# Kernel optimization log

Hardware: AMD Instinct MI355X
Metric: run time of the kernel (lower is better)

The kernel has to match this reference:

```python
import jax, jax.numpy as jnp
import numpy as np

B, N, NODE_DIM = 256, 200, 2
H, D, L, FF = 8, 128, 3, 512
KD = D // H  # key/val dim per head = 16
EPS = 1e-5


def _uniform(key, shape, fan):
    s = 1.0 / np.sqrt(fan)
    return jax.random.uniform(key, shape, jnp.float32, -s, s)


def setup_inputs() -> dict:
    key = jax.random.key(0)
    ks = jax.random.split(key, 16)
    return {
        "x": jax.random.normal(ks[0], (B, N, NODE_DIM), jnp.float32),
        "Wemb": _uniform(ks[1], (NODE_DIM, D), NODE_DIM),
        "bemb": _uniform(ks[2], (D,), NODE_DIM),
        "Wq": _uniform(ks[3], (L, H, D, KD), KD),
        "Wk": _uniform(ks[4], (L, H, D, KD), KD),
        "Wv": _uniform(ks[5], (L, H, D, KD), KD),
        "Wo": _uniform(ks[6], (L, H, KD, D), D),
        "bn1_g": jnp.ones((L, D), jnp.float32),
        "bn1_b": jnp.zeros((L, D), jnp.float32),
        "W1": _uniform(ks[7], (L, D, FF), D),
        "b1": _uniform(ks[8], (L, FF), D),
        "W2": _uniform(ks[9], (L, FF, D), FF),
        "b2": _uniform(ks[10], (L, D), FF),
        "bn2_g": jnp.ones((L, D), jnp.float32),
        "bn2_b": jnp.zeros((L, D), jnp.float32),
    }


def _batch_norm(h, g, b):
    # BatchNorm1d in training mode: stats over all (batch*graph) positions per channel
    hf = h.reshape(-1, h.shape[-1])
    m = hf.mean(axis=0)
    v = hf.var(axis=0)  # biased variance, as torch uses for normalization
    return (h - m) * jax.lax.rsqrt(v + EPS) * g + b


def _mha(h, Wq, Wk, Wv, Wo):
    # h: [B,N,D]; Wq/Wk/Wv: [H,D,KD]; Wo: [H,KD,D]
    Q = jnp.einsum('bnd,hdk->hbnk', h, Wq)
    K = jnp.einsum('bnd,hdk->hbnk', h, Wk)
    V = jnp.einsum('bnd,hdk->hbnk', h, Wv)
    scores = jnp.einsum('hbqk,hbnk->hbqn', Q, K) * (1.0 / np.sqrt(KD))
    attn = jax.nn.softmax(scores, axis=-1)
    heads = jnp.einsum('hbqn,hbnk->hbqk', attn, V)
    return jnp.einsum('hbqk,hkd->bqd', heads, Wo)


def reference(x, Wemb, bemb, Wq, Wk, Wv, Wo, bn1_g, bn1_b, W1, b1, W2, b2, bn2_g, bn2_b):
    h = x @ Wemb + bemb  # init_embed: [B,N,D]
    for l in range(L):
        h = h + _mha(h, Wq[l], Wk[l], Wv[l], Wo[l])
        h = _batch_norm(h, bn1_g[l], bn1_b[l])
        ff = jax.nn.relu(h @ W1[l] + b1[l]) @ W2[l] + b2[l]
        h = _batch_norm(h + ff, bn2_g[l], bn2_b[l])
    return (h, h.mean(axis=1))
```

## Files before the change

### kernel.cpp

```cpp
#include <hip/hip_runtime.h>
#include <math.h>

#define B_ 256
#define N_ 200
#define D_ 128
#define H_ 8
#define KD_ 16
#define L_ 3
#define FF_ 512
#define ROWS (B_*N_)
#define BND (ROWS*D_)

typedef float f32x4 __attribute__((ext_vector_type(4)));
typedef _Float16 f16x4 __attribute__((ext_vector_type(4)));
typedef _Float16 f16x8 __attribute__((ext_vector_type(8)));

__device__ __forceinline__ ushort f2h_bits(float f) {
  _Float16 h = (_Float16)f;
  union { _Float16 h; ushort u; } v; v.h = h; return v.u;
}
__device__ __forceinline__ float h2f(ushort u) {
  union { ushort u; _Float16 h; } v; v.u = u; return (float)v.h;
}
__device__ __forceinline__ void bn_reduce(const float* psum, const float* psq,
    const float* gamma, const float* beta, int c, float& sc, float& sh) {
  if (gamma == nullptr) { sc = 1.f; sh = 0.f; return; }
  float s = psum[c], q = psq[c];
  const float invM = 1.f / 51200.f;
  float m = s * invM;
  float v = fmaf(q, invM, -m * m);
  float rr = rsqrtf(v + 1e-5f);
  sc = rr * gamma[c];
  sh = fmaf(-m, sc, beta[c]);
}

__global__ __launch_bounds__(256) void init_kernel(const float* __restrict__ x,
    const float* __restrict__ Wemb, const float* __restrict__ bemb,
    const float* __restrict__ Wo, const float* __restrict__ W2,
    ushort* __restrict__ h, ushort* __restrict__ woT, ushort* __restrict__ w2T,
    float* __restrict__ pa_s, float* __restrict__ pa_q,
    float* __restrict__ pb_s, float* __restrict__ pb_q)
{
  int blk = blockIdx.x, t = threadIdx.x;
  if (blk < 6400) {
    int i4 = blk * 256 + t;
    int r  = i4 >> 5, c4 = i4 & 31;
    float x0 = x[2*r], x1 = x[2*r + 1];
    const float4 w0 = ((const float4*)Wemb)[c4];
    const float4 w1 = ((const float4*)Wemb)[32 + c4];
    const float4 bb = ((const float4*)bemb)[c4];
    ushort o16[4];
    o16[0] = f2h_bits(fmaf(x0, w0.x, fmaf(x1, w1.x, bb.x)));
    o16[1] = f2h_bits(fmaf(x0, w0.y, fmaf(x1, w1.y, bb.y)));
    o16[2] = f2h_bits(fmaf(x0, w0.z, fmaf(x1, w1.z, bb.z)));
    o16[3] = f2h_bits(fmaf(x0, w0.w, fmaf(x1, w1.w, bb.w)));
    uint2 p;
    p.x = (uint)o16[0] | ((uint)o16[1] << 16);
    p.y = (uint)o16[2] | ((uint)o16[3] << 16);
    ((uint2*)h)[i4] = p;
  } else if (blk < 7360) {
    int i = (blk - 6400) * 256 + t;
    if (i < 49152) {
      int l = i / 16384, r = i % 16384;
      int n = r >> 7, k = r & 127;
      int hh = k >> 4, kd = k & 15;
      woT[i] = f2h_bits(Wo[l*16384 + hh*2048 + kd*128 + n]);
    } else {
      int j = i - 49152;
      int l = j / 65536, r = j % 65536;
      int d = r >> 9, f = r & 511;
      w2T[j] = f2h_bits(W2[l*65536 + f*128 + d]);
    }
  } else {
    if (t < 128) { pa_s[t] = 0.f; pa_q[t] = 0.f; pb_s[t] = 0.f; pb_q[t] = 0.f; }
  }
}

__global__ __launch_bounds__(128) void fold_qkv(const float* __restrict__ Wq,
    const float* __restrict__ Wk, const float* __restrict__ Wv,
    const float* __restrict__ pb_s, const float* __restrict__ pb_q,
    const float* __restrict__ gamma, const float* __restrict__ beta,
    ushort* __restrict__ wh, float* __restrict__ bout,
    float* __restrict__ scout, float* __restrict__ shout,
    float* __restrict__ pa_s, float* __restrict__ pa_q)
{
  __shared__ float wsum[2];
  int n = blockIdx.x;
  int k = threadIdx.x;
  float sc, sh;
  bn_reduce(pb_s, pb_q, gamma, beta, k, sc, sh);
  if (n == 0) { scout[k] = sc; shout[k] = sh; }
  if (n == 1) { pa_s[k] = 0.f; pa_q[k] = 0.f; }
  int which = n >> 7, hh = (n >> 4) & 7, kd = n & 15;
  const float* src = (which == 0) ? Wq : (which == 1) ? Wk : Wv;
  float w = src[hh*2048 + k*16 + kd];
  if (which == 0) w *= 0.25f * 1.44269504088896340736f;
  wh[n*128 + k] = f2h_bits(w * sc);
  float p = sh * w;
#pragma unroll
  for (int d = 1; d < 64; d <<= 1) p += __shfl_xor(p, d);
  if ((k & 63) == 0) wsum[k >> 6] = p;
  __syncthreads();
  if (k == 0) bout[n] = wsum[0] + wsum[1];
}

__global__ __launch_bounds__(128) void fold_w1(const float* __restrict__ W1,
    const float* __restrict__ b1,
    const float* __restrict__ pa_s, const float* __restrict__ pa_q,
    const float* __restrict__ gamma, const float* __restrict__ beta,
    ushort* __restrict__ wh, float* __restrict__ bout,
    float* __restrict__ scout, float* __restrict__ shout)
{
  __shared__ float wsum[2];
  int f = blockIdx.x;
  int k = threadIdx.x;
  float sc, sh;
  bn_reduce(pa_s, pa_q, gamma, beta, k, sc, sh);
  if (f == 0) { scout[k] = sc; shout[k] = sh; }
  float w = W1[k*512 + f];
  wh[f*128 + k] = f2h_bits(w * sc);
  float p = sh * w;
#pragma unroll
  for (int d = 1; d < 64; d <<= 1) p += __shfl_xor(p, d);
  if ((k & 63) == 0) wsum[k >> 6] = p;
  __syncthreads();
  if (k == 0) bout[f] = b1[f] + wsum[0] + wsum[1];
}

template<int K, bool BIAS, bool RELU, bool RESIDBN,
         bool OUTQKV, bool OUT16, bool STATS>
__global__ __launch_bounds__(256, 2) void gemm_mfma(
    const ushort* __restrict__ Ah,
    const ushort* __restrict__ Wh,
    const float* __restrict__ bias,
    const ushort* rh,
    const float* __restrict__ rsc, const float* __restrict__ rsh,
    ushort* o0, ushort* o1, ushort* o2,
    float* __restrict__ psum, float* __restrict__ psq, int Ntot)
{
  __shared__ ushort AhS[128*64];
  __shared__ ushort BhS[128*64];
  const int t    = threadIdx.x;
  const int nx   = gridDim.x;
  const int nwg  = nx * gridDim.y;
  const int lin  = blockIdx.y * nx + blockIdx.x;
  const int q8   = nwg >> 3, r8 = nwg & 7;
  const int xcd  = lin & 7, i8 = lin >> 3;
  const int wg   = (xcd < r8 ? xcd*(q8+1) : r8*(q8+1) + (xcd-r8)*q8) + i8;
  const int bm   = (wg / nx) * 128;
  const int bn   = (wg % nx) * 128;
  const int lane = t & 63;
  const int w    = t >> 6, wm = w >> 1, wn = w & 1;
  const int quad = lane >> 4, l15 = lane & 15;

  f32x4 acc[4][4];
#pragma unroll
  for (int i = 0; i < 4; i++)
#pragma unroll
    for (int j = 0; j < 4; j++) acc[i][j] = (f32x4){0.f, 0.f, 0.f, 0.f};

  const ushort* AhB = Ah + (size_t)bm * K;
  const ushort* BhB = Wh + (size_t)bn * K;

  for (int k0 = 0; k0 < K; k0 += 64) {
#pragma unroll
    for (int i = 0; i < 4; i++) {
      int idx = i * 256 + t;
      int row = idx >> 3, c = idx & 7;
      int k8  = c ^ (row & 7);
      size_t off = (size_t)row * K + k0 + k8 * 8;
      ((uint4*)AhS)[idx] = *(const uint4*)(AhB + off);
      ((uint4*)BhS)[idx] = *(const uint4*)(BhB + off);
    }
    __syncthreads();
#pragma unroll
    for (int ks = 0; ks < 2; ks++) {
      f16x8 ah[4], bh[4];
#pragma unroll
      for (int i = 0; i < 4; i++) {
        int row = wm * 64 + i * 16 + l15;
        int k8  = ks * 4 + quad;
        int ci  = k8 ^ (row & 7);
        ah[i] = ((const f16x8*)AhS)[row * 8 + ci];
        int nrow = wn * 64 + i * 16 + l15;
        int cj   = k8 ^ (nrow & 7);
        bh[i] = ((const f16x8*)BhS)[nrow * 8 + cj];
      }
#pragma unroll
      for (int i = 0; i < 4; i++)
#pragma unroll
        for (int j = 0; j < 4; j++)
          acc[i][j] = __builtin_amdgcn_mfma_f32_16x16x32_f16(ah[i], bh[j], acc[i][j], 0, 0, 0);
    }
    __syncthreads();
  }

  float bv[4], scv[4], shv[4];
#pragma unroll
  for (int j = 0; j < 4; j++) {
    int col = bn + wn*64 + j*16 + l15;
    if (BIAS)    bv[j]  = bias[col];
    if (RESIDBN) { scv[j] = rsc[col]; shv[j] = rsh[col]; }
  }
  float sj[4] = {0.f,0.f,0.f,0.f}, qj[4] = {0.f,0.f,0.f,0.f};
#pragma unroll
  for (int i = 0; i < 4; i++) {
#pragma unroll
    for (int r = 0; r < 4; r++) {
      int row = bm + wm*64 + i*16 + quad*4 + r;
#pragma unroll
      for (int j = 0; j < 4; j++) {
        int col = bn + wn*64 + j*16 + l15;
        float v = acc[i][j][r];
        if (BIAS)    v += bv[j];
        if (RELU)    v = fmaxf(v, 0.f);
        if (RESIDBN) {
          float rr = h2f(rh[(size_t)row * Ntot + col]);
          v += fmaf(rr, scv[j], shv[j]);
        }
        if (OUTQKV) {
          if (bn == 0) {
            o0[((size_t)(col >> 4) * ROWS + row) * 16 + (col & 15)] = f2h_bits(v);
          } else if (bn == 128) {
            int c = col - 128;
            o1[((size_t)(c >> 4) * ROWS + row) * 16 + (c & 15)] = f2h_bits(v);
          } else {
            int c = col - 256;
            o2[((size_t)(c >> 4) * ROWS + row) * 16 + (c & 15)] = f2h_bits(v);
          }
        }
        if (OUT16) o0[(size_t)row * Ntot + col] = f2h_bits(v);
        if (STATS) { sj[j] += v; qj[j] = fmaf(v, v, qj[j]); }
      }
    }
  }
  if (STATS) {
#pragma unroll
    for (int j = 0; j < 4; j++) {
      sj[j] += __shfl_xor(sj[j], 16); sj[j] += __shfl_xor(sj[j], 32);
      qj[j] += __shfl_xor(qj[j], 16); qj[j] += __shfl_xor(qj[j], 32);
    }
    float* ssum = (float*)AhS;
    float* ssq  = ssum + 128;
    if (t < 128) { ssum[t] = 0.f; ssq[t] = 0.f; }
    __syncthreads();
    if (quad == 0) {
#pragma unroll
      for (int j = 0; j < 4; j++) {
        int col = wn*64 + j*16 + l15;
        atomicAdd(&ssum[col], sj[j]);
        atomicAdd(&ssq[col],  qj[j]);
      }
    }
    __syncthreads();
    if (t < 128) {
      atomicAdd(&psum[t], ssum[t]);
      atomicAdd(&psq[t],  ssq[t]);
    }
  }
}

__global__ __launch_bounds__(256) void attn_kernel(const ushort* __restrict__ qs,
    const ushort* __restrict__ ks, const ushort* __restrict__ vh,
    ushort* __restrict__ hd, float* __restrict__ pb_s, float* __restrict__ pb_q)
{
  __shared__ __align__(16) _Float16 Ksh[208*24];
  __shared__ __align__(16) _Float16 VTh[16*216];
  const int b  = blockIdx.x >> 3;
  const int hh = blockIdx.x & 7;
  const int t  = threadIdx.x;
  if (blockIdx.x == 0 && t < 128) { pb_s[t] = 0.f; pb_q[t] = 0.f; }
  const size_t rb = (size_t)b * N_;
  const size_t hb = ((size_t)hh * ROWS + rb) * 16;

  for (int i = t; i < 208*2; i += 256) {
    int n = i >> 1, half = i & 1;
    uint4 kv = {0u, 0u, 0u, 0u};
    if (n < N_) kv = *(const uint4*)(ks + hb + n*16 + half*8);
    *(uint4*)&Ksh[n*24 + half*8] = kv;
  }
  for (int i = t; i < 208*2; i += 256) {
    int n = i >> 1, half = i & 1;
    uint4 v0 = {0u, 0u, 0u, 0u};
    if (n < N_) v0 = *(const uint4*)(vh + hb + n*16 + half*8);
    const ushort* e0 = (const ushort*)&v0;
#pragma unroll
    for (int q = 0; q < 8; q++)
      ((ushort*)VTh)[(half*8 + q)*216 + n] = e0[q];
  }
  __syncthreads();

  const int lane = t & 63;
  const int w    = t >> 6;
  const int l15  = lane & 15;
  const int g    = lane >> 4;

  for (int qt = w; qt < 13; qt += 4) {
    int qr  = qt*16 + l15;
    int qrc = qr < N_ ? qr : N_-1;
    f16x4 bq = *(const f16x4*)(qs + hb + (size_t)qrc*16 + g*4);

    f32x4 ct[13];
#pragma unroll
    for (int kt = 0; kt < 13; kt++) {
      f16x4 ak = *(const f16x4*)&Ksh[(kt*16 + l15)*24 + g*4];
      ct[kt] = __builtin_amdgcn_mfma_f32_16x16x16f16(ak, bq, (f32x4){0.f,0.f,0.f,0.f}, 0, 0, 0);
    }
#pragma unroll
    for (int r = 0; r < 4; r++)
      if (g*4 + r >= 8) ct[12][r] = -1e30f;

    float m0 = -1e30f, m1 = -1e30f;
#pragma unroll
    for (int kt = 0; kt < 13; kt++) {
      m0 = fmaxf(m0, fmaxf(ct[kt][0], ct[kt][1]));
      m1 = fmaxf(m1, fmaxf(ct[kt][2], ct[kt][3]));
    }
    float m = fmaxf(m0, m1);
    m = fmaxf(m, __shfl_xor(m, 16));
    m = fmaxf(m, __shfl_xor(m, 32));

    float la0 = 0.f, la1 = 0.f, la2 = 0.f, la3 = 0.f;
#pragma unroll
    for (int kt = 0; kt < 13; kt++) {
      float p0 = __builtin_amdgcn_exp2f(ct[kt][0] - m);
      float p1 = __builtin_amdgcn_exp2f(ct[kt][1] - m);
      float p2 = __builtin_amdgcn_exp2f(ct[kt][2] - m);
      float p3 = __builtin_amdgcn_exp2f(ct[kt][3] - m);
      la0 += p0; la1 += p1; la2 += p2; la3 += p3;
      ct[kt][0] = p0; ct[kt][1] = p1; ct[kt][2] = p2; ct[kt][3] = p3;
    }
    float l = (la0 + la1) + (la2 + la3);
    l += __shfl_xor(l, 16);
    l += __shfl_xor(l, 32);

    f32x4 och = {0.f,0.f,0.f,0.f};
#pragma unroll
    for (int kt = 0; kt < 13; kt++) {
      f16x4 pt = { (_Float16)ct[kt][0], (_Float16)ct[kt][1],
                   (_Float16)ct[kt][2], (_Float16)ct[kt][3] };
      f16x4 avh = *(const f16x4*)&VTh[l15*216 + kt*16 + g*4];
      och = __builtin_amdgcn_mfma_f32_16x16x16f16(avh, pt, och, 0, 0, 0);
    }

    if (qr < N_) {
      float inv = __builtin_amdgcn_rcpf(l);
      ushort o16[4];
#pragma unroll
      for (int r = 0; r < 4; r++) o16[r] = f2h_bits(och[r] * inv);
      uint2 p;
      p.x = (uint)o16[0] | ((uint)o16[1] << 16);
      p.y = (uint)o16[2] | ((uint)o16[3] << 16);
      *(uint2*)(hd + (rb + qr)*128 + hh*16 + g*4) = p;
    }
  }
}

__global__ __launch_bounds__(256) void bn_mean_final(const ushort* __restrict__ h,
    const float* __restrict__ pb_s, const float* __restrict__ pb_q,
    const float* __restrict__ gamma, const float* __restrict__ beta,
    float* __restrict__ outh, float* __restrict__ mout)
{
  __shared__ float part[2][128];
  int b = blockIdx.x;
  int t = threadIdx.x;
  int d = t & 127, half = t >> 7;
  float sc, sh;
  bn_reduce(pb_s, pb_q, gamma, beta, d, sc, sh);
  float s = 0.f;
  for (int n = half*100; n < half*100 + 100; n++) {
    size_t idx = ((size_t)b * N_ + n) * 128 + d;
    float v = fmaf(h2f(h[idx]), sc, sh);
    outh[idx] = v;
    s += v;
  }
  part[half][d] = s;
  __syncthreads();
  if (half == 0) mout[b * 128 + d] = (part[0][d] + part[1][d]) * (1.f / N_);
}

extern "C" void kernel_launch(void* const* d_in, const int* in_sizes, int n_in,
                              void* d_out, int out_size, void* d_ws, size_t ws_size,
                              hipStream_t stream)
{
  const float* x    = (const float*)d_in[0];
  const float* Wemb = (const float*)d_in[1];
  const float* bemb = (const float*)d_in[2];
  const float* Wq   = (const float*)d_in[3];
  const float* Wk   = (const float*)d_in[4];
  const float* Wv   = (const float*)d_in[5];
  const float* Wo   = (const float*)d_in[6];
  const float* bn1g = (const float*)d_in[7];
  const float* bn1b = (const float*)d_in[8];
  const float* W1   = (const float*)d_in[9];
  const float* b1   = (const float*)d_in[10];
  const float* W2   = (const float*)d_in[11];
  const float* b2   = (const float*)d_in[12];
  const float* bn2g = (const float*)d_in[13];
  const float* bn2b = (const float*)d_in[14];
  float* out = (float*)d_out;

  char* wsb = (char*)d_ws;
  ushort* h     = (ushort*)wsb;
  char*   phase = wsb + 13107200;
  ushort* qsb   = (ushort*)phase;
  ushort* ksb   = (ushort*)(phase + 13107200);
  ushort* vhh   = (ushort*)(phase + 26214400);
  ushort* hd    = (ushort*)(phase + 52428800);
  ushort* hid   = (ushort*)phase;
  char*   wp    = wsb + 78643200;
  ushort* woT   = (ushort*)wp;
  ushort* w2T   = (ushort*)(wp + 98304);
  ushort* fqkvw = (ushort*)(wp + 491520);
  ushort* fw1w  = (ushort*)(wp + 589824);
  float*  fqkv_b = (float*)(wp + 720896);
  float*  fw1_b  = (float*)(wp + 722432);
  float*  pa_s   = (float*)(wp + 724480);
  float*  pa_q   = (float*)(wp + 724992);
  float*  pb_s   = (float*)(wp + 725504);
  float*  pb_q   = (float*)(wp + 726016);
  float*  sc_a   = (float*)(wp + 726528);
  float*  sh_a   = (float*)(wp + 727040);
  float*  sc_b   = (float*)(wp + 727552);
  float*  sh_b   = (float*)(wp + 728064);

  init_kernel<<<7361, 256, 0, stream>>>(x, Wemb, bemb, Wo, W2, h, woT, w2T,
                                        pa_s, pa_q, pb_s, pb_q);

  for (int l = 0; l < L_; l++) {
    fold_qkv<<<384, 128, 0, stream>>>(Wq + l*16384, Wk + l*16384, Wv + l*16384,
                                      pb_s, pb_q,
                                      l == 0 ? nullptr : bn2g + (l-1)*128,
                                      l == 0 ? nullptr : bn2b + (l-1)*128,
                                      fqkvw, fqkv_b, sc_b, sh_b, pa_s, pa_q);
    gemm_mfma<128, true, false, false, true, false, false>
        <<<dim3(3, 400), 256, 0, stream>>>(
        h, fqkvw, fqkv_b, nullptr, nullptr, nullptr,
        qsb, ksb, vhh, nullptr, nullptr, 384);
    attn_kernel<<<B_ * H_, 256, 0, stream>>>(qsb, ksb, vhh, hd, pb_s, pb_q);
    gemm_mfma<128, false, false, true, false, true, true>
        <<<dim3(1, 400), 256, 0, stream>>>(
        hd, woT + l*16384, nullptr, h, sc_b, sh_b,
        h, nullptr, nullptr, pa_s, pa_q, 128);
    fold_w1<<<512, 128, 0, stream>>>(W1 + l*65536, b1 + l*512,
                                     pa_s, pa_q, bn1g + l*128, bn1b + l*128,
                                     fw1w, fw1_b, sc_a, sh_a);
    gemm_mfma<128, true, true, false, false, true, false>
        <<<dim3(4, 400), 256, 0, stream>>>(
        h, fw1w, fw1_b, nullptr, nullptr, nullptr,
        hid, nullptr, nullptr, nullptr, nullptr, 512);
    gemm_mfma<512, true, false, true, false, true, true>
        <<<dim3(1, 400), 256, 0, stream>>>(
        hid, w2T + l*65536, b2 + l*128, h, sc_a, sh_a,
        h, nullptr, nullptr, pb_s, pb_q, 128);
  }

  bn_mean_final<<<B_, 256, 0, stream>>>(h, pb_s, pb_q,
                                        bn2g + 2*128, bn2b + 2*128, out, out + BND);
}
```

Before: 527.7 us.

## Fuse FFN up- and down-projection GEMMs into one kernel keeping hidden tile in LDS

Replaces the two FFN GEMM launches (W1 with ReLU writing a 512-wide hidden activation to global memory, then W2 reading it back) with a single kernel. Each 128-row block loops over four 128-wide hidden chunks, computes relu(h·W1+b1) into shared memory and immediately accumulates it into the W2 output. The same kernel also applies the residual with BN scale/shift and accumulates BN statistics. This removes the global round trip of the hidden tensor and one launch, but there are only 400 blocks at one block per CU with about 96KB of LDS each, so per-CU occupancy is low and weight loads are not double-buffered.

After: 552.1 us. 4.6% more time.

```diff
diff --git a/kernel.cpp b/kernel.cpp
--- a/kernel.cpp
+++ b/kernel.cpp
@@ -260,6 +260,187 @@
   }
 }
 
+__global__ __launch_bounds__(256, 1) void ffn_fused(
+    const ushort* __restrict__ h,
+    const ushort* __restrict__ w1,
+    const float* __restrict__ b1f,
+    const ushort* __restrict__ w2t,
+    const float* __restrict__ b2,
+    const float* __restrict__ rsc, const float* __restrict__ rsh,
+    ushort* hout,
+    float* __restrict__ psum, float* __restrict__ psq)
+{
+  __shared__ ushort Ash[2*128*64];
+  __shared__ ushort WB [2*128*64];
+  __shared__ ushort HB [2*128*72];
+  const int t    = threadIdx.x;
+  const int bm   = blockIdx.x * 128;
+  const int lane = t & 63;
+  const int w    = t >> 6, wm = w >> 1, wn = w & 1;
+  const int quad = lane >> 4, l15 = lane & 15;
+
+  {
+    const ushort* AB = h + (size_t)bm * 128;
+    for (int half = 0; half < 2; half++)
+#pragma unroll
+      for (int i = 0; i < 4; i++) {
+        int idx = i * 256 + t;
+        int row = idx >> 3, c = idx & 7;
+        int k8  = c ^ (row & 7);
+        ((uint4*)(Ash + half*8192))[idx] = *(const uint4*)(AB + (size_t)row*128 + half*64 + k8*8);
+      }
+  }
+
+  f32x4 aco[4][4];
+#pragma unroll
+  for (int i = 0; i < 4; i++)
+#pragma unroll
+    for (int j = 0; j < 4; j++) aco[i][j] = (f32x4){0.f, 0.f, 0.f, 0.f};
+
+  __syncthreads();
+
+  for (int ch = 0; ch < 4; ch++) {
+    {
+      const ushort* W1B = w1 + (size_t)ch * 128 * 128;
+      for (int half = 0; half < 2; half++)
+#pragma unroll
+        for (int i = 0; i < 4; i++) {
+          int idx = i * 256 + t;
+          int row = idx >> 3, c = idx & 7;
+          int k8  = c ^ (row & 7);
+          ((uint4*)(WB + half*8192))[idx] = *(const uint4*)(W1B + (size_t)row*128 + half*64 + k8*8);
+        }
+    }
+    __syncthreads();
+    f32x4 ach[4][4];
+#pragma unroll
+    for (int i = 0; i < 4; i++)
+#pragma unroll
+      for (int j = 0; j < 4; j++) ach[i][j] = (f32x4){0.f, 0.f, 0.f, 0.f};
+#pragma unroll
+    for (int ks = 0; ks < 4; ks++) {
+      int half = ks >> 1, k8 = (ks & 1)*4 + quad;
+      f16x8 ah[4], bh[4];
+#pragma unroll
+      for (int i = 0; i < 4; i++) {
+        int row = wm*64 + i*16 + l15;
+        int ci  = k8 ^ (row & 7);
+        ah[i] = ((const f16x8*)(Ash + half*8192))[row*8 + ci];
+        int fr = wn*64 + i*16 + l15;
+        int cj  = k8 ^ (fr & 7);
+        bh[i] = ((const f16x8*)(WB + half*8192))[fr*8 + cj];
+      }
+#pragma unroll
+      for (int i = 0; i < 4; i++)
+#pragma unroll
+        for (int j = 0; j < 4; j++)
+          ach[i][j] = __builtin_amdgcn_mfma_f32_16x16x32_f16(ah[i], bh[j], ach[i][j], 0, 0, 0);
+    }
+    __syncthreads();
+    {
+      float bv1[4];
+#pragma unroll
+      for (int j = 0; j < 4; j++) bv1[j] = b1f[ch*128 + wn*64 + j*16 + l15];
+#pragma unroll
+      for (int i = 0; i < 4; i++)
+#pragma unroll
+        for (int r = 0; r < 4; r++) {
+          int row = wm*64 + i*16 + quad*4 + r;
+#pragma unroll
+          for (int j = 0; j < 4; j++) {
+            float hv = fmaxf(ach[i][j][r] + bv1[j], 0.f);
+            int k6  = j*16 + l15;
+            int ci8 = (k6 >> 3) ^ (row & 7);
+            HB[(wn*128 + row)*72 + ci8*8 + (l15 & 7)] = f2h_bits(hv);
+          }
+        }
+    }
+    {
+      const ushort* W2B = w2t + ch * 128;
+      for (int half = 0; half < 2; half++)
+#pragma unroll
+        for (int i = 0; i < 4; i++) {
+          int idx = i * 256 + t;
+          int row = idx >> 3, c = idx & 7;
+          int k8  = c ^ (row & 7);
+          ((uint4*)(WB + half*8192))[idx] = *(const uint4*)(W2B + (size_t)row*512 + half*64 + k8*8);
+        }
+    }
+    __syncthreads();
+#pragma unroll
+    for (int ks = 0; ks < 4; ks++) {
+      int half = ks >> 1, k8 = (ks & 1)*4 + quad;
+      f16x8 ah[4], bh[4];
+#pragma unroll
+      for (int i = 0; i < 4; i++) {
+        int row = wm*64 + i*16 + l15;
+        int ci  = k8 ^ (row & 7);
+        ah[i] = *(const f16x8*)&HB[(half*128 + row)*72 + ci*8];
+        int dr = wn*64 + i*16 + l15;
+        int cj  = k8 ^ (dr & 7);
+        bh[i] = ((const f16x8*)(WB + half*8192))[dr*8 + cj];
+      }
+#pragma unroll
+      for (int i = 0; i < 4; i++)
+#pragma unroll
+        for (int j = 0; j < 4; j++)
+          aco[i][j] = __builtin_amdgcn_mfma_f32_16x16x32_f16(ah[i], bh[j], aco[i][j], 0, 0, 0);
+    }
+    __syncthreads();
+  }
+
+  float bv[4], scv[4], shv[4];
+#pragma unroll
+  for (int j = 0; j < 4; j++) {
+    int col = wn*64 + j*16 + l15;
+    bv[j]  = b2[col];
+    scv[j] = rsc[col]; shv[j] = rsh[col];
+  }
+  float sj[4] = {0.f,0.f,0.f,0.f}, qj[4] = {0.f,0.f,0.f,0.f};
+#pragma unroll
+  for (int i = 0; i < 4; i++) {
+#pragma unroll
+    for (int r = 0; r < 4; r++) {
+      int rloc = wm*64 + i*16 + quad*4 + r;
+      int row  = bm + rloc;
+#pragma unroll
+      for (int j = 0; j < 4; j++) {
+        int col = wn*64 + j*16 + l15;
+        float v = aco[i][j][r] + bv[j];
+        int k6 = col & 63, half = col >> 6;
+        int ci = (k6 >> 3) ^ (rloc & 7);
+        float rr = h2f(Ash[half*8192 + rloc*64 + ci*8 + (k6 & 7)]);
+        v += fmaf(rr, scv[j], shv[j]);
+        hout[(size_t)row * 128 + col] = f2h_bits(v);
+        sj[j] += v; qj[j] = fmaf(v, v, qj[j]);
+      }
+    }
+  }
+#pragma unroll
+  for (int j = 0; j < 4; j++) {
+    sj[j] += __shfl_xor(sj[j], 16); sj[j] += __shfl_xor(sj[j], 32);
+    qj[j] += __shfl_xor(qj[j], 16); qj[j] += __shfl_xor(qj[j], 32);
+  }
+  __syncthreads();
+  float* ssum = (float*)Ash;
+  float* ssq  = ssum + 128;
+  if (t < 128) { ssum[t] = 0.f; ssq[t] = 0.f; }
+  __syncthreads();
+  if (quad == 0) {
+#pragma unroll
+    for (int j = 0; j < 4; j++) {
+      int col = wn*64 + j*16 + l15;
+      atomicAdd(&ssum[col], sj[j]);
+      atomicAdd(&ssq[col],  qj[j]);
+    }
+  }
+  __syncthreads();
+  if (t < 128) {
+    atomicAdd(&psum[t], ssum[t]);
+    atomicAdd(&psq[t],  ssq[t]);
+  }
+}
+
 __global__ __launch_bounds__(256) void attn_kernel(const ushort* __restrict__ qs,
     const ushort* __restrict__ ks, const ushort* __restrict__ vh,
     ushort* __restrict__ hd, float* __restrict__ pb_s, float* __restrict__ pb_q)
@@ -406,9 +587,8 @@
   ushort* qsb   = (ushort*)phase;
   ushort* ksb   = (ushort*)(phase + 13107200);
   ushort* vhh   = (ushort*)(phase + 26214400);
-  ushort* hd    = (ushort*)(phase + 52428800);
-  ushort* hid   = (ushort*)phase;
-  char*   wp    = wsb + 78643200;
+  ushort* hd    = (ushort*)(phase + 39321600);
+  char*   wp    = wsb + 65536000;
   ushort* woT   = (ushort*)wp;
   ushort* w2T   = (ushort*)(wp + 98304);
   ushort* fqkvw = (ushort*)(wp + 491520);
@@ -445,14 +625,9 @@
     fold_w1<<<512, 128, 0, stream>>>(W1 + l*65536, b1 + l*512,
                                      pa_s, pa_q, bn1g + l*128, bn1b + l*128,
                                      fw1w, fw1_b, sc_a, sh_a);
-    gemm_mfma<128, true, true, false, false, true, false>
-        <<<dim3(4, 400), 256, 0, stream>>>(
-        h, fw1w, fw1_b, nullptr, nullptr, nullptr,
-        hid, nullptr, nullptr, nullptr, nullptr, 512);
-    gemm_mfma<512, true, false, true, false, true, true>
-        <<<dim3(1, 400), 256, 0, stream>>>(
-        hid, w2T + l*65536, b2 + l*128, h, sc_a, sh_a,
-        h, nullptr, nullptr, pb_s, pb_q, 128);
+    ffn_fused<<<400, 256, 0, stream>>>(
+        h, fw1w, fw1_b, w2T + l*65536, b2 + l*128, sc_a, sh_a,
+        h, pb_s, pb_q);
   }
 
   bn_mean_final<<<B_, 256, 0, stream>>>(h, pb_s, pb_q,
```

## Fuse FFN up- and down-projection GEMMs into one kernel keeping hidden in registers

Applied to the files above, without the earlier changes.

Replaces the two FFN GEMM launches (W1 with ReLU writing a 512-wide fp16 hidden buffer, then W2 with residual, BN-apply and stats) with a single kernel. Each block handles 64 rows, loops over four 128-wide hidden chunks, and stages swizzled W1 and W2 tiles in shared memory. The hidden activations stay in registers as fp16 MFMA operands and are never written to global memory. This saves the hidden tensor's write and read traffic and one launch, but weights are reloaded per 64-row block and reuse per block is lower, and the input h is read and written in place.

New measurement: 592.8 us. 1.12x slower.

```diff
diff --git a/kernel.cpp b/kernel.cpp
--- a/kernel.cpp
+++ b/kernel.cpp
@@ -260,6 +260,129 @@
   }
 }
 
+__global__ __launch_bounds__(256, 3) void ffn_fused(
+    const ushort* __restrict__ h,
+    const ushort* __restrict__ w1,
+    const float* __restrict__ b1f,
+    const ushort* __restrict__ w2t,
+    const float* __restrict__ b2,
+    const float* __restrict__ rsc, const float* __restrict__ rsh,
+    ushort* hout,
+    float* __restrict__ psum, float* __restrict__ psq)
+{
+  __shared__ ushort WB[128*128];
+  __shared__ float ssum[128], ssq[128];
+  const int t    = threadIdx.x;
+  const int bm   = blockIdx.x * 64;
+  const int lane = t & 63;
+  const int wv   = t >> 6;
+  const int quad = lane >> 4, l15 = lane & 15;
+  const int row  = bm + wv*16 + l15;
+
+  f16x4 bq[8];
+#pragma unroll
+  for (int ks = 0; ks < 8; ks++)
+    bq[ks] = *(const f16x4*)(h + (size_t)row*128 + ks*16 + quad*4);
+
+  if (t < 128) { ssum[t] = 0.f; ssq[t] = 0.f; }
+
+  f32x4 co[8];
+#pragma unroll
+  for (int dt = 0; dt < 8; dt++) co[dt] = (f32x4){0.f,0.f,0.f,0.f};
+
+  for (int ch = 0; ch < 4; ch++) {
+    __syncthreads();
+    {
+      const ushort* W1B = w1 + (size_t)ch*128*128;
+#pragma unroll
+      for (int i = 0; i < 8; i++) {
+        int idx = i*256 + t;
+        int r = idx >> 4, c = idx & 15;
+        int k8 = c ^ (r & 7);
+        ((uint4*)WB)[idx] = *(const uint4*)(W1B + (size_t)r*128 + k8*8);
+      }
+    }
+    __syncthreads();
+    f16x4 hb[8];
+#pragma unroll
+    for (int ft = 0; ft < 8; ft++) {
+      f32x4 hc = (f32x4){0.f,0.f,0.f,0.f};
+#pragma unroll
+      for (int ks = 0; ks < 8; ks++) {
+        int fr = ft*16 + l15;
+        int k  = ks*16 + quad*4;
+        int gi = (k >> 3) ^ (fr & 7);
+        f16x4 af = *(const f16x4*)&WB[fr*128 + gi*8 + (k & 7)];
+        hc = __builtin_amdgcn_mfma_f32_16x16x16f16(af, bq[ks], hc, 0, 0, 0);
+      }
+      float4 b1v = *(const float4*)(b1f + ch*128 + ft*16 + quad*4);
+      hb[ft] = (f16x4){
+        (_Float16)fmaxf(hc[0] + b1v.x, 0.f),
+        (_Float16)fmaxf(hc[1] + b1v.y, 0.f),
+        (_Float16)fmaxf(hc[2] + b1v.z, 0.f),
+        (_Float16)fmaxf(hc[3] + b1v.w, 0.f) };
+    }
+    __syncthreads();
+    {
+      const ushort* W2B = w2t + ch*128;
+#pragma unroll
+      for (int i = 0; i < 8; i++) {
+        int idx = i*256 + t;
+        int r = idx >> 4, c = idx & 15;
+        int k8 = c ^ (r & 7);
+        ((uint4*)WB)[idx] = *(const uint4*)(W2B + (size_t)r*512 + k8*8);
+      }
+    }
+    __syncthreads();
+#pragma unroll
+    for (int dt = 0; dt < 8; dt++) {
+#pragma unroll
+      for (int ft = 0; ft < 8; ft++) {
+        int dr = dt*16 + l15;
+        int k  = ft*16 + quad*4;
+        int gi = (k >> 3) ^ (dr & 7);
+        f16x4 af = *(const f16x4*)&WB[dr*128 + gi*8 + (k & 7)];
+        co[dt] = __builtin_amdgcn_mfma_f32_16x16x16f16(af, hb[ft], co[dt], 0, 0, 0);
+      }
+    }
+  }
+
+#pragma unroll
+  for (int dt = 0; dt < 8; dt++) {
+    int d0 = dt*16 + quad*4;
+    float4 b2v = *(const float4*)(b2 + d0);
+    float4 scv = *(const float4*)(rsc + d0);
+    float4 shv = *(const float4*)(rsh + d0);
+    f16x4 rr = *(const f16x4*)(h + (size_t)row*128 + d0);
+    float v0 = co[dt][0] + b2v.x + fmaf((float)rr[0], scv.x, shv.x);
+    float v1 = co[dt][1] + b2v.y + fmaf((float)rr[1], scv.y, shv.y);
+    float v2 = co[dt][2] + b2v.z + fmaf((float)rr[2], scv.z, shv.z);
+    float v3 = co[dt][3] + b2v.w + fmaf((float)rr[3], scv.w, shv.w);
+    f16x4 ov = { (_Float16)v0, (_Float16)v1, (_Float16)v2, (_Float16)v3 };
+    *(f16x4*)(hout + (size_t)row*128 + d0) = ov;
+    float s0 = v0, s1 = v1, s2 = v2, s3 = v3;
+    float q0 = v0*v0, q1 = v1*v1, q2 = v2*v2, q3 = v3*v3;
+#pragma unroll
+    for (int m = 1; m < 16; m <<= 1) {
+      s0 += __shfl_xor(s0, m); s1 += __shfl_xor(s1, m);
+      s2 += __shfl_xor(s2, m); s3 += __shfl_xor(s3, m);
+      q0 += __shfl_xor(q0, m); q1 += __shfl_xor(q1, m);
+      q2 += __shfl_xor(q2, m); q3 += __shfl_xor(q3, m);
+    }
+    if (l15 == 0) {
+      atomicAdd(&ssum[d0+0], s0); atomicAdd(&ssum[d0+1], s1);
+      atomicAdd(&ssum[d0+2], s2); atomicAdd(&ssum[d0+3], s3);
+      atomicAdd(&ssq[d0+0], q0);  atomicAdd(&ssq[d0+1], q1);
+      atomicAdd(&ssq[d0+2], q2);  atomicAdd(&ssq[d0+3], q3);
+    }
+  }
+  __syncthreads();
+  if (t < 128) {
+    atomicAdd(&psum[t], ssum[t]);
+    atomicAdd(&psq [t], ssq [t]);
+  }
+}
+
 __global__ __launch_bounds__(256) void attn_kernel(const ushort* __restrict__ qs,
     const ushort* __restrict__ ks, const ushort* __restrict__ vh,
     ushort* __restrict__ hd, float* __restrict__ pb_s, float* __restrict__ pb_q)
@@ -406,9 +529,8 @@
   ushort* qsb   = (ushort*)phase;
   ushort* ksb   = (ushort*)(phase + 13107200);
   ushort* vhh   = (ushort*)(phase + 26214400);
-  ushort* hd    = (ushort*)(phase + 52428800);
-  ushort* hid   = (ushort*)phase;
-  char*   wp    = wsb + 78643200;
+  ushort* hd    = (ushort*)(phase + 39321600);
+  char*   wp    = wsb + 65536000;
   ushort* woT   = (ushort*)wp;
   ushort* w2T   = (ushort*)(wp + 98304);
   ushort* fqkvw = (ushort*)(wp + 491520);
@@ -445,14 +567,9 @@
     fold_w1<<<512, 128, 0, stream>>>(W1 + l*65536, b1 + l*512,
                                      pa_s, pa_q, bn1g + l*128, bn1b + l*128,
                                      fw1w, fw1_b, sc_a, sh_a);
-    gemm_mfma<128, true, true, false, false, true, false>
-        <<<dim3(4, 400), 256, 0, stream>>>(
-        h, fw1w, fw1_b, nullptr, nullptr, nullptr,
-        hid, nullptr, nullptr, nullptr, nullptr, 512);
-    gemm_mfma<512, true, false, true, false, true, true>
-        <<<dim3(1, 400), 256, 0, stream>>>(
-        hid, w2T + l*65536, b2 + l*128, h, sc_a, sh_a,
-        h, nullptr, nullptr, pb_s, pb_q, 128);
+    ffn_fused<<<800, 256, 0, stream>>>(
+        h, fw1w, fw1_b, w2T + l*65536, b2 + l*128, sc_a, sh_a,
+        h, pb_s, pb_q);
   }
 
   bn_mean_final<<<B_, 256, 0, stream>>>(h, pb_s, pb_q,
```
